# Kernel optimization log

Measured on AMD Instinct MI355X. Metric: run time of the kernel, lower is better.

## Reference

```python
import jax, jax.numpy as jnp
import numpy as np

B, S, D = 8, 4096, 1024
H, DH = 16, 64
DM = H * DH  # d_model = 1024


def setup_inputs() -> dict:
    key = jax.random.key(0)
    k0, k1, k2, k3 = jax.random.split(key, 4)
    x = jax.random.uniform(k0, (B, S, D), dtype=jnp.float32)
    # nn.Linear weights (stored here pre-transposed as [in, out]).
    Wq = jax.random.normal(k1, (D, DM), dtype=jnp.float32) * 0.02
    Wkv = jax.random.normal(k2, (D, 2 * DM), dtype=jnp.float32) * 0.02
    Wlin = jax.random.normal(k3, (DM, DM), dtype=jnp.float32) * 0.02
    blin = jnp.zeros((DM,), dtype=jnp.float32)
    return {"x": x, "Wq": Wq, "Wkv": Wkv, "Wlin": Wlin, "blin": blin}


def reference(x, Wq, Wkv, Wlin, blin):
    scale = DH ** (-0.5)
    # projections; cond_dim=None => cond = x (self attention), mask=None
    q = (x @ Wq).reshape(B, S, H, DH)          # [B,S,H,DH]
    kv = (x @ Wkv).reshape(B, S, H, 2 * DH)    # [B,S,H,2*DH]
    k, v = kv[..., :DH], kv[..., DH:]
    # dual softmax: q over feature dim (scaled), k over sequence dim
    q = jax.nn.softmax(q, axis=-1) * scale
    k = jax.nn.softmax(k, axis=1)              # seq axis in BSHD layout
    # context = k^T @ v per (batch, head): [B,H,DH,DH]
    context = jnp.einsum('bshd,bshe->bhde', k, v)
    # out = q @ context: [B,S,H,DH]
    out = jnp.einsum('bshd,bhde->bshe', q, context).reshape(B, S, DM)
    return out @ Wlin + blin
```

## Files before the change

### kernel.cpp

```cpp
#include <hip/hip_runtime.h>
#include <hip/hip_bf16.h>
#include <cstdint>

using bf16 = __hip_bfloat16;
typedef __attribute__((ext_vector_type(8))) short bf16x8;
typedef __attribute__((ext_vector_type(4))) float f32x4;

struct alignas(16) B8 { bf16 h[8]; };
struct alignas(8)  B4 { bf16 h[4]; };

__device__ __forceinline__ void gll16(const void* g, void* l) {
  __builtin_amdgcn_global_load_lds((__attribute__((address_space(1))) void*)g,
                                   (__attribute__((address_space(3))) void*)l,
                                   16, 0, 0);
}


__global__ __launch_bounds__(256) void cast_x_frag(const float* __restrict__ x,
                                                   bf16* __restrict__ xr) {
  __shared__ float tile[16][257];
  const int g = blockIdx.x;
  const int t = threadIdx.x;
  const float* src = x + (size_t)g * 16384;
  bf16* dst = xr + (size_t)g * 16384;
  const int r = t >> 4, cl = t & 15;
  for (int kp = 0; kp < 4; ++kp) {
    const int k0 = kp * 256;
    if (kp) __syncthreads();
    #pragma unroll
    for (int s = 0; s < 4; ++s) {
      const int c0 = cl * 4 + 64 * s;
      float4 v = *(const float4*)(src + (size_t)r * 1024 + k0 + c0);
      tile[r][c0 + 0] = v.x; tile[r][c0 + 1] = v.y;
      tile[r][c0 + 2] = v.z; tile[r][c0 + 3] = v.w;
    }
    __syncthreads();
    #pragma unroll
    for (int rd = 0; rd < 2; ++rd) {
      const int c = rd * 256 + t;
      const int ql = c >> 4, rr = c & 15;
      B8 o;
      #pragma unroll
      for (int jj = 0; jj < 8; ++jj) o.h[jj] = __float2bfloat16(tile[rr][ql * 8 + jj]);
      *(B8*)(dst + ((size_t)(kp * 32 + ql) * 16 + rr) * 8) = o;
    }
  }
}

__global__ __launch_bounds__(256) void wcast_frag(const float* __restrict__ W,
                                                  bf16* __restrict__ out,
                                                  int N, int n_glob0) {
  __shared__ float tw[256][17];
  const int k0 = blockIdx.x * 256;
  const int n0 = blockIdx.y * 16;
  const int t = threadIdx.x;
  {
    const int nn = t & 15, kk0 = t >> 4;
    #pragma unroll
    for (int s = 0; s < 16; ++s) {
      const int kk = kk0 + 16 * s;
      tw[kk][nn] = W[(size_t)(k0 + kk) * N + n0 + nn];
    }
  }
  __syncthreads();
  const int ng = (n_glob0 + n0) >> 4;
  #pragma unroll
  for (int rd = 0; rd < 2; ++rd) {
    const int c = rd * 256 + t;
    const int ql = c >> 4, r = c & 15;
    B8 o;
    #pragma unroll
    for (int jj = 0; jj < 8; ++jj) o.h[jj] = __float2bfloat16(tw[ql * 8 + jj][r]);
    *(B8*)(out + (((size_t)ng * 128 + (k0 >> 3) + ql) * 16 + r) * 8) = o;
  }
}

__global__ void tcast(const float* __restrict__ W, bf16* __restrict__ WT, int K, int N) {
  __shared__ float tile[32][33];
  int k0 = blockIdx.y * 32, n0 = blockIdx.x * 32;
  int tx = threadIdx.x, ty = threadIdx.y;
  for (int yy = ty; yy < 32; yy += 8)
    tile[yy][tx] = W[(size_t)(k0 + yy) * N + n0 + tx];
  __syncthreads();
  for (int yy = ty; yy < 32; yy += 8)
    WT[(size_t)(n0 + yy) * K + k0 + tx] = __float2bfloat16(tile[tx][yy]);
}

__device__ __forceinline__ void gemm_mainloop_256(
    const bf16* __restrict__ aop0, const bf16* __restrict__ aop1,
    const bf16* __restrict__ bop0, const bf16* __restrict__ bop1,
    bf16* ldsA, bf16* ldsB, int wd0, int wd1,
    int aoff, int boff, f32x4 (&acc)[8][4])
{
#define STAGE_A(slot, ko) do { gll16(aop0 + (ko) * 16, ldsA + (slot) * 8192 + wd0); \
                               gll16(aop1 + (ko) * 16, ldsA + (slot) * 8192 + wd1); } while (0)
#define STAGE_B(slot, ko) do { gll16(bop0 + (ko) * 16, ldsB + (slot) * 8192 + wd0); \
                               gll16(bop1 + (ko) * 16, ldsB + (slot) * 8192 + wd1); } while (0)
#define AFRAG(slot, i) (*(const bf16x8*)(ldsA + (slot) * 8192 + aoff + (i) * 512))
#define BFRAG(slot, j) (*(const bf16x8*)(ldsB + (slot) * 8192 + boff + (j) * 512))

  bf16x8 a1[4], a2[4], bb[2][4];

#define SECTION(S, CURB, NXTB, DO_PF, PFS, DO_ST, SLOT, KO)                         \
  do {                                                                              \
    asm volatile("s_waitcnt lgkmcnt(0)" ::: "memory");                              \
    __builtin_amdgcn_sched_barrier(0);                                              \
    __builtin_amdgcn_s_setprio(1);                                                  \
    _Pragma("unroll")                                                               \
    for (int i = 0; i < 4; i++) {                                                   \
      _Pragma("unroll")                                                             \
      for (int j = 0; j < 4; j++)                                                   \
        acc[i][j] = __builtin_amdgcn_mfma_f32_16x16x32_bf16(a1[i], bb[CURB][j],     \
                                                            acc[i][j], 0, 0, 0);    \
      a2[i] = AFRAG(S, i + 4);                                                      \
      if (DO_ST && i == 0) gll16(aop0 + (KO) * 16, ldsA + (SLOT) * 8192 + wd0);     \
      if (DO_ST && i == 1) gll16(aop1 + (KO) * 16, ldsA + (SLOT) * 8192 + wd1);     \
    }                                                                               \
    asm volatile("s_waitcnt lgkmcnt(0)" ::: "memory");                              \
    __builtin_amdgcn_sched_barrier(0);                                              \
    _Pragma("unroll")                                                               \
    for (int i = 0; i < 4; i++) {                                                   \
      _Pragma("unroll")                                                             \
      for (int j = 0; j < 4; j++)                                                   \
        acc[i + 4][j] = __builtin_amdgcn_mfma_f32_16x16x32_bf16(a2[i], bb[CURB][j], \
                                                                acc[i + 4][j], 0, 0, 0); \
      if (DO_PF) { bb[NXTB][i] = BFRAG(PFS, i); a1[i] = AFRAG(PFS, i); }            \
      if (DO_ST && i == 0) gll16(bop0 + (KO) * 16, ldsB + (SLOT) * 8192 + wd0);     \
      if (DO_ST && i == 1) gll16(bop1 + (KO) * 16, ldsB + (SLOT) * 8192 + wd1);     \
    }                                                                               \
    __builtin_amdgcn_s_setprio(0);                                                  \
  } while (0)

#define BOUNDARY(VMC)                                                               \
  do {                                                                              \
    asm volatile("s_waitcnt vmcnt(" #VMC ")" ::: "memory");                         \
    __builtin_amdgcn_s_barrier();                                                   \
    __builtin_amdgcn_sched_barrier(0);                                              \
  } while (0)

  STAGE_A(0, 0);  STAGE_B(0, 0);
  STAGE_A(1, 32); STAGE_B(1, 32);
  STAGE_A(2, 64); STAGE_B(2, 64);
  asm volatile("s_waitcnt vmcnt(4)" ::: "memory");
  __builtin_amdgcn_s_barrier();
  __builtin_amdgcn_sched_barrier(0);
  #pragma unroll
  for (int j = 0; j < 4; j++) bb[0][j] = BFRAG(0, j);
  #pragma unroll
  for (int i = 0; i < 4; i++) a1[i] = AFRAG(0, i);

  for (int q = 0; q < 7; ++q) {
    const int ko = q * 128;
    SECTION(0, 0, 1, true, 1, true, 3, ko + 96);
    BOUNDARY(4);
    SECTION(1, 1, 0, true, 2, true, 0, ko + 128);
    BOUNDARY(4);
    SECTION(2, 0, 1, true, 3, true, 1, ko + 160);
    BOUNDARY(4);
    SECTION(3, 1, 0, true, 0, true, 2, ko + 192);
    BOUNDARY(4);
  }
  SECTION(0, 0, 1, true, 1, true, 3, 992);
  BOUNDARY(4);
  SECTION(1, 1, 0, true, 2, false, 0, 0);
  BOUNDARY(0);
  SECTION(2, 0, 1, true, 3, false, 0, 0);
  BOUNDARY(0);
  SECTION(3, 1, 0, false, 0, false, 0, 0);

  __syncthreads();
#undef SECTION
#undef BOUNDARY
#undef STAGE_A
#undef STAGE_B
#undef AFRAG
#undef BFRAG
}

constexpr int QKV_NT = 12;

__global__ __launch_bounds__(512, 2)
void gemm_qkv(const bf16* __restrict__ A, const bf16* __restrict__ BT,
              bf16* __restrict__ Yq, float* __restrict__ ctxAcc)
{
  __shared__ __align__(16) union {
    struct { bf16 a[4 * 8192]; bf16 b[4 * 8192]; } g;
    struct { bf16 ekT[2][16384]; bf16 vT[2][16384]; } c;
  } sm;

  const int t = threadIdx.x;
  const int wave = t >> 6, lane = t & 63;
  const int lr = lane & 15, kq = lane >> 4;
  const int wm = wave >> 2, wn = wave & 3;
  const int bid = (int)blockIdx.x;
  const int swz = (bid & 7) * 192 + (bid >> 3);
  const int bm = swz / QKV_NT, bn = swz % QKV_NT;
  const int m0 = bm * 256, n0 = bn * 256;

  const bf16* aop0 = A + (size_t)((m0 >> 4) + wave) * 16384 + lane * 8;
  const bf16* aop1 = aop0 + 131072;
  const bf16* bop0 = BT + (size_t)((n0 >> 4) + wave) * 16384 + lane * 8;
  const bf16* bop1 = bop0 + 131072;
  const int wd0 = wave * 512;
  const int wd1 = 4096 + wave * 512;

  const int aoff = wm * 4096 + lane * 8;
  const int boff = wn * 2048 + lane * 8;

  const f32x4 zero = {0.f, 0.f, 0.f, 0.f};
  f32x4 acc[8][4];
  #pragma unroll
  for (int i = 0; i < 8; i++)
    #pragma unroll
    for (int j = 0; j < 4; j++) acc[i][j] = zero;

  gemm_mainloop_256(aop0, aop1, bop0, bop1, sm.g.a, sm.g.b, wd0, wd1,
                    aoff, boff, acc);

  if (bn < 4) {
    const int qb = (n0 + wn * 64) >> 3;
    const int jo = (lr >> 3) * 128;
    #pragma unroll
    for (int i = 0; i < 8; i++) {
      #pragma unroll
      for (int r = 0; r < 4; r++) {
        float m = fmaxf(fmaxf(acc[i][0][r], acc[i][1][r]),
                        fmaxf(acc[i][2][r], acc[i][3][r]));
        m = fmaxf(m, __shfl_xor(m, 1));
        m = fmaxf(m, __shfl_xor(m, 2));
        m = fmaxf(m, __shfl_xor(m, 4));
        m = fmaxf(m, __shfl_xor(m, 8));
        float ex[4]; float s = 0.f;
        #pragma unroll
        for (int j = 0; j < 4; j++) { ex[j] = __expf(acc[i][j][r] - m); s += ex[j]; }
        s += __shfl_xor(s, 1);
        s += __shfl_xor(s, 2);
        s += __shfl_xor(s, 4);
        s += __shfl_xor(s, 8);
        const float inv = 0.125f / s;
        const int row = m0 + wm * 128 + i * 16 + kq * 4 + r;
        bf16* yb = Yq + (((size_t)(row >> 4) * 128 + qb) * 16 + (row & 15)) * 8 + (lr & 7);
        #pragma unroll
        for (int j = 0; j < 4; j++)
          yb[j * 256 + jo] = __float2bfloat16(ex[j] * inv);
      }
    }
  } else {
    const int bb2 = m0 >> 12;
    const int h0 = (n0 - 1024) >> 7;
    const int hloc = wn >> 1, isV = wn & 1;
    bf16* const dstT = (isV ? sm.c.vT[hloc] : sm.c.ekT[hloc]);

    float zp[4] = {0.f, 0.f, 0.f, 0.f};
    #pragma unroll
    for (int i = 0; i < 8; i++) {
      const int sbase = wm * 128 + i * 16 + kq * 4;
      const int sxo = sbase >> 3;
      const int sby = (sbase & 7) * 2;
      #pragma unroll
      for (int j = 0; j < 4; j++) {
        const int d = j * 16 + lr;
        B4 pk;
        if (!isV) {
          #pragma unroll
          for (int r = 0; r < 4; r++) {
            float e = __expf(acc[i][j][r]);
            zp[j] += e;
            pk.h[r] = __float2bfloat16(e);
          }
        } else {
          #pragma unroll
          for (int r = 0; r < 4; r++) pk.h[r] = __float2bfloat16(acc[i][j][r]);
        }
        *(B4*)((char*)dstT + d * 512 + ((sxo ^ (d & 7)) << 4) + sby) = pk;
      }
    }

    if (!isV) {
      #pragma unroll
      for (int j = 0; j < 4; j++) {
        zp[j] += __shfl_xor(zp[j], 16);
        zp[j] += __shfl_xor(zp[j], 32);
      }
      if (kq == 0) {
        float* zb = ctxAcc + (size_t)(bb2 * 16 + h0 + hloc) * 4160 + 4096;
        #pragma unroll
        for (int j = 0; j < 4; j++) atomicAdd(zb + j * 16 + lr, zp[j]);
      }
    }
    __syncthreads();

    const int hh = wave >> 2, dq = wave & 3;
    const bf16* const ek = sm.c.ekT[hh];
    const bf16* const vv = sm.c.vT[hh];
    f32x4 racc[4] = {zero, zero, zero, zero};
    #pragma unroll
    for (int ks = 0; ks < 8; ks++) {
      const int ch = ks * 4 + kq;
      bf16x8 af = *(const bf16x8*)((const char*)ek + (dq * 16 + lr) * 512 + ((ch ^ (lr & 7)) << 4));
      #pragma unroll
      for (int j = 0; j < 4; j++) {
        bf16x8 bfr = *(const bf16x8*)((const char*)vv + (j * 16 + lr) * 512 + ((ch ^ (lr & 7)) << 4));
        racc[j] = __builtin_amdgcn_mfma_f32_16x16x32_bf16(af, bfr, racc[j], 0, 0, 0);
      }
    }
    float* cb = ctxAcc + (size_t)(bb2 * 16 + h0 + hh) * 4160;
    #pragma unroll
    for (int j = 0; j < 4; j++) {
      #pragma unroll
      for (int r = 0; r < 4; r++)
        atomicAdd(cb + (dq * 16 + kq * 4 + r) * 64 + j * 16 + lr, racc[j][r]);
    }
  }
}

__global__ __launch_bounds__(256) void make_w2t(const float* __restrict__ ctxAcc,
                                                const bf16* __restrict__ WlinT,
                                                bf16* __restrict__ W2T) {
  const int nc = blockIdx.x;
  const int bh = blockIdx.y;
  const int b = bh >> 4, h = bh & 15;
  const int t = threadIdx.x, lane = t & 63, w = t >> 6;
  const float* src = ctxAcc + (size_t)bh * 4160;
  const float invz = 1.0f / src[4096 + lane];
  float creg[64];
  const float* crow = src + lane * 64;
  #pragma unroll
  for (int e4 = 0; e4 < 16; e4++) {
    float4 v = *(const float4*)(crow + e4 * 4);
    creg[e4 * 4 + 0] = v.x * invz; creg[e4 * 4 + 1] = v.y * invz;
    creg[e4 * 4 + 2] = v.z * invz; creg[e4 * 4 + 3] = v.w * invz;
  }
  for (int i = 0; i < 16; i++) {
    const int n = nc * 64 + w * 16 + i;
    const bf16* wrow = WlinT + (size_t)n * 1024 + h * 64;
    float acc = 0.f;
    #pragma unroll
    for (int e8 = 0; e8 < 8; e8++) {
      B8 v = *(const B8*)(wrow + e8 * 8);
      #pragma unroll
      for (int j = 0; j < 8; j++) acc += creg[e8 * 8 + j] * __bfloat162float(v.h[j]);
    }
    W2T[(size_t)b * 1048576 +
        (((size_t)(n >> 4) * 128 + h * 8 + (lane >> 3)) * 16 + (n & 15)) * 8 + (lane & 7)]
        = __float2bfloat16(acc);
  }
}

__global__ __launch_bounds__(512, 2)
void gemm_out(const bf16* __restrict__ Aall, const bf16* __restrict__ BTall,
              float* __restrict__ Call, const float* __restrict__ bias)
{
  __shared__ __align__(16) struct { bf16 a[4 * 8192]; bf16 b[4 * 8192]; } sm;
  const int t = threadIdx.x;
  const int wave = t >> 6, lane = t & 63;
  const int lr = lane & 15, kq = lane >> 4;
  const int wm = wave >> 2, wn = wave & 3;
  const int bid = (int)blockIdx.x;
  const int swz = (bid & 7) * 64 + (bid >> 3);
  const int bz = swz >> 6;
  const int r  = swz & 63;
  const int bm = r >> 2, bn = r & 3;
  const int m0 = bm * 256, n0 = bn * 256;
  const bf16* A  = Aall  + (size_t)bz * 4194304;
  const bf16* BT = BTall + (size_t)bz * 1048576;
  float* C       = Call  + (size_t)bz * 4194304;

  const bf16* aop0 = A + (size_t)((m0 >> 4) + wave) * 16384 + lane * 8;
  const bf16* aop1 = aop0 + 131072;
  const bf16* bop0 = BT + (size_t)((n0 >> 4) + wave) * 16384 + lane * 8;
  const bf16* bop1 = bop0 + 131072;
  const int wd0 = wave * 512;
  const int wd1 = 4096 + wave * 512;

  const int aoff = wm * 4096 + lane * 8;
  const int boff = wn * 2048 + lane * 8;

  const f32x4 zero = {0.f, 0.f, 0.f, 0.f};
  f32x4 acc[8][4];
  #pragma unroll
  for (int i = 0; i < 8; i++)
    #pragma unroll
    for (int j = 0; j < 4; j++) acc[i][j] = zero;

  gemm_mainloop_256(aop0, aop1, bop0, bop1, sm.a, sm.b, wd0, wd1,
                    aoff, boff, acc);

  float bv[4];
  #pragma unroll
  for (int j = 0; j < 4; j++) bv[j] = bias[n0 + wn * 64 + j * 16 + lr];
  #pragma unroll
  for (int i = 0; i < 8; i++) {
    const int row0 = m0 + wm * 128 + i * 16 + kq * 4;
    #pragma unroll
    for (int j = 0; j < 4; j++) {
      const int col = n0 + wn * 64 + j * 16 + lr;
      const float bvj = bv[j];
      #pragma unroll
      for (int r2 = 0; r2 < 4; r2++)
        C[(size_t)(row0 + r2) * 1024 + col] = acc[i][j][r2] + bvj;
    }
  }
}

extern "C" void kernel_launch(void* const* d_in, const int* in_sizes, int n_in,
                              void* d_out, int out_size, void* d_ws, size_t ws_size,
                              hipStream_t stream) {
  (void)in_sizes; (void)n_in; (void)out_size; (void)ws_size;
  const float* x    = (const float*)d_in[0];
  const float* Wq   = (const float*)d_in[1];
  const float* Wkv  = (const float*)d_in[2];
  const float* Wlin = (const float*)d_in[3];
  const float* blin = (const float*)d_in[4];
  float* out = (float*)d_out;

  bf16* x_bf  = (bf16*)d_ws;
  bf16* WTc   = x_bf + 33554432;
  bf16* WlinT = WTc + 3145728;
  bf16* Yq    = WlinT + 1048576;
  bf16* W2T   = Yq + 33554432;
  float* ctxAcc = (float*)(W2T + 8388608);

  cast_x_frag<<<2048, 256, 0, stream>>>(x, x_bf);
  wcast_frag<<<dim3(4, 64), 256, 0, stream>>>(Wq, WTc, 1024, 0);
  wcast_frag<<<dim3(4, 128), 256, 0, stream>>>(Wkv, WTc, 2048, 1024);
  tcast<<<dim3(32, 32), dim3(32, 8), 0, stream>>>(Wlin, WlinT, 1024, 1024);

  hipMemsetAsync(ctxAcc, 0, (size_t)128 * 4160 * sizeof(float), stream);

  gemm_qkv<<<dim3(128 * QKV_NT), 512, 0, stream>>>(x_bf, WTc, Yq, ctxAcc);
  make_w2t<<<dim3(16, 128), 256, 0, stream>>>(ctxAcc, WlinT, W2T);
  gemm_out<<<dim3(512), 512, 0, stream>>>(Yq, W2T, out, blin);
}
```

Baseline: 370.2 us.

## Load GEMM B fragments directly from global into registers, bypassing LDS

The shared GEMM mainloop no longer stages the B operand through LDS. Each wave now reads its B fragments straight from global memory into registers, one K-step ahead, and the vmcnt waits are adjusted to cover these loads. This halves LDS use and removes B's LDS traffic, which could allow more occupancy. In exchange, the four waves sharing each N-column re-read B from global/L2, and B-load latency now sits in the MFMA pipeline with only one step of lookahead.

New measurement: 368.2 us. About the same (-0.5%).

```diff
diff --git a/kernel.cpp b/kernel.cpp
--- a/kernel.cpp
+++ b/kernel.cpp
@@ -88,20 +88,17 @@
 
 __device__ __forceinline__ void gemm_mainloop_256(
     const bf16* __restrict__ aop0, const bf16* __restrict__ aop1,
-    const bf16* __restrict__ bop0, const bf16* __restrict__ bop1,
-    bf16* ldsA, bf16* ldsB, int wd0, int wd1,
-    int aoff, int boff, f32x4 (&acc)[8][4])
+    const bf16* __restrict__ bfp,
+    bf16* ldsA, int wd0, int wd1, int aoff, f32x4 (&acc)[8][4])
 {
 #define STAGE_A(slot, ko) do { gll16(aop0 + (ko) * 16, ldsA + (slot) * 8192 + wd0); \
                                gll16(aop1 + (ko) * 16, ldsA + (slot) * 8192 + wd1); } while (0)
-#define STAGE_B(slot, ko) do { gll16(bop0 + (ko) * 16, ldsB + (slot) * 8192 + wd0); \
-                               gll16(bop1 + (ko) * 16, ldsB + (slot) * 8192 + wd1); } while (0)
 #define AFRAG(slot, i) (*(const bf16x8*)(ldsA + (slot) * 8192 + aoff + (i) * 512))
-#define BFRAG(slot, j) (*(const bf16x8*)(ldsB + (slot) * 8192 + boff + (j) * 512))
+#define BGLOB(j, ko) (*(const bf16x8*)(bfp + (size_t)(j) * 16384 + (ko) * 16))
 
   bf16x8 a1[4], a2[4], bb[2][4];
 
-#define SECTION(S, CURB, NXTB, DO_PF, PFS, DO_ST, SLOT, KO)                         \
+#define SECTION(S, CURB, NXTB, DO_PFB, BKO, DO_PF, PFS, DO_ST, SLOT, KO)            \
   do {                                                                              \
     asm volatile("s_waitcnt lgkmcnt(0)" ::: "memory");                              \
     __builtin_amdgcn_sched_barrier(0);                                              \
@@ -115,6 +112,7 @@
       a2[i] = AFRAG(S, i + 4);                                                      \
       if (DO_ST && i == 0) gll16(aop0 + (KO) * 16, ldsA + (SLOT) * 8192 + wd0);     \
       if (DO_ST && i == 1) gll16(aop1 + (KO) * 16, ldsA + (SLOT) * 8192 + wd1);     \
+      if (DO_PFB) bb[NXTB][i] = BGLOB(i, BKO);                                      \
     }                                                                               \
     asm volatile("s_waitcnt lgkmcnt(0)" ::: "memory");                              \
     __builtin_amdgcn_sched_barrier(0);                                              \
@@ -124,9 +122,7 @@
       for (int j = 0; j < 4; j++)                                                   \
         acc[i + 4][j] = __builtin_amdgcn_mfma_f32_16x16x32_bf16(a2[i], bb[CURB][j], \
                                                                 acc[i + 4][j], 0, 0, 0); \
-      if (DO_PF) { bb[NXTB][i] = BFRAG(PFS, i); a1[i] = AFRAG(PFS, i); }            \
-      if (DO_ST && i == 0) gll16(bop0 + (KO) * 16, ldsB + (SLOT) * 8192 + wd0);     \
-      if (DO_ST && i == 1) gll16(bop1 + (KO) * 16, ldsB + (SLOT) * 8192 + wd1);     \
+      if (DO_PF) { a1[i] = AFRAG(PFS, i); }                                         \
     }                                                                               \
     __builtin_amdgcn_s_setprio(0);                                                  \
   } while (0)
@@ -138,43 +134,41 @@
     __builtin_amdgcn_sched_barrier(0);                                              \
   } while (0)
 
-  STAGE_A(0, 0);  STAGE_B(0, 0);
-  STAGE_A(1, 32); STAGE_B(1, 32);
-  STAGE_A(2, 64); STAGE_B(2, 64);
+  STAGE_A(0, 0); STAGE_A(1, 32); STAGE_A(2, 64);
+  #pragma unroll
+  for (int j = 0; j < 4; j++) bb[0][j] = BGLOB(j, 0);
   asm volatile("s_waitcnt vmcnt(4)" ::: "memory");
   __builtin_amdgcn_s_barrier();
   __builtin_amdgcn_sched_barrier(0);
   #pragma unroll
-  for (int j = 0; j < 4; j++) bb[0][j] = BFRAG(0, j);
-  #pragma unroll
   for (int i = 0; i < 4; i++) a1[i] = AFRAG(0, i);
 
   for (int q = 0; q < 7; ++q) {
     const int ko = q * 128;
-    SECTION(0, 0, 1, true, 1, true, 3, ko + 96);
-    BOUNDARY(4);
-    SECTION(1, 1, 0, true, 2, true, 0, ko + 128);
-    BOUNDARY(4);
-    SECTION(2, 0, 1, true, 3, true, 1, ko + 160);
-    BOUNDARY(4);
-    SECTION(3, 1, 0, true, 0, true, 2, ko + 192);
-    BOUNDARY(4);
-  }
-  SECTION(0, 0, 1, true, 1, true, 3, 992);
-  BOUNDARY(4);
-  SECTION(1, 1, 0, true, 2, false, 0, 0);
-  BOUNDARY(0);
-  SECTION(2, 0, 1, true, 3, false, 0, 0);
-  BOUNDARY(0);
-  SECTION(3, 1, 0, false, 0, false, 0, 0);
-
+    SECTION(0, 0, 1, true, ko + 32,  true, 1, true, 3, ko + 96);
+    BOUNDARY(6);
+    SECTION(1, 1, 0, true, ko + 64,  true, 2, true, 0, ko + 128);
+    BOUNDARY(6);
+    SECTION(2, 0, 1, true, ko + 96,  true, 3, true, 1, ko + 160);
+    BOUNDARY(6);
+    SECTION(3, 1, 0, true, ko + 128, true, 0, true, 2, ko + 192);
+    BOUNDARY(6);
+  }
+  SECTION(0, 0, 1, true, 928, true, 1, true, 3, 992);
+  BOUNDARY(6);
+  SECTION(1, 1, 0, true, 960, true, 2, false, 0, 0);
+  BOUNDARY(6);
+  SECTION(2, 0, 1, true, 992, true, 3, false, 0, 0);
+  BOUNDARY(6);
+  SECTION(3, 1, 0, false, 0, false, 0, false, 0, 0);
+
+  asm volatile("s_waitcnt vmcnt(0)" ::: "memory");
   __syncthreads();
 #undef SECTION
 #undef BOUNDARY
 #undef STAGE_A
-#undef STAGE_B
 #undef AFRAG
-#undef BFRAG
+#undef BGLOB
 }
 
 constexpr int QKV_NT = 12;
@@ -184,7 +178,7 @@
               bf16* __restrict__ Yq, float* __restrict__ ctxAcc)
 {
   __shared__ __align__(16) union {
-    struct { bf16 a[4 * 8192]; bf16 b[4 * 8192]; } g;
+    struct { bf16 a[4 * 8192]; } g;
     struct { bf16 ekT[2][16384]; bf16 vT[2][16384]; } c;
   } sm;
 
@@ -199,13 +193,10 @@
 
   const bf16* aop0 = A + (size_t)((m0 >> 4) + wave) * 16384 + lane * 8;
   const bf16* aop1 = aop0 + 131072;
-  const bf16* bop0 = BT + (size_t)((n0 >> 4) + wave) * 16384 + lane * 8;
-  const bf16* bop1 = bop0 + 131072;
+  const bf16* bfp = BT + (size_t)((n0 >> 4) + wn * 4) * 16384 + lane * 8;
   const int wd0 = wave * 512;
   const int wd1 = 4096 + wave * 512;
-
   const int aoff = wm * 4096 + lane * 8;
-  const int boff = wn * 2048 + lane * 8;
 
   const f32x4 zero = {0.f, 0.f, 0.f, 0.f};
   f32x4 acc[8][4];
@@ -214,8 +205,7 @@
     #pragma unroll
     for (int j = 0; j < 4; j++) acc[i][j] = zero;
 
-  gemm_mainloop_256(aop0, aop1, bop0, bop1, sm.g.a, sm.g.b, wd0, wd1,
-                    aoff, boff, acc);
+  gemm_mainloop_256(aop0, aop1, bfp, sm.g.a, wd0, wd1, aoff, acc);
 
   if (bn < 4) {
     const int qb = (n0 + wn * 64) >> 3;
@@ -351,7 +341,7 @@
 void gemm_out(const bf16* __restrict__ Aall, const bf16* __restrict__ BTall,
               float* __restrict__ Call, const float* __restrict__ bias)
 {
-  __shared__ __align__(16) struct { bf16 a[4 * 8192]; bf16 b[4 * 8192]; } sm;
+  __shared__ __align__(16) struct { bf16 a[4 * 8192]; } sm;
   const int t = threadIdx.x;
   const int wave = t >> 6, lane = t & 63;
   const int lr = lane & 15, kq = lane >> 4;
@@ -368,13 +358,10 @@
 
   const bf16* aop0 = A + (size_t)((m0 >> 4) + wave) * 16384 + lane * 8;
   const bf16* aop1 = aop0 + 131072;
-  const bf16* bop0 = BT + (size_t)((n0 >> 4) + wave) * 16384 + lane * 8;
-  const bf16* bop1 = bop0 + 131072;
+  const bf16* bfp = BT + (size_t)((n0 >> 4) + wn * 4) * 16384 + lane * 8;
   const int wd0 = wave * 512;
   const int wd1 = 4096 + wave * 512;
-
   const int aoff = wm * 4096 + lane * 8;
-  const int boff = wn * 2048 + lane * 8;
 
   const f32x4 zero = {0.f, 0.f, 0.f, 0.f};
   f32x4 acc[8][4];
@@ -383,8 +370,7 @@
     #pragma unroll
     for (int j = 0; j < 4; j++) acc[i][j] = zero;
 
-  gemm_mainloop_256(aop0, aop1, bop0, bop1, sm.a, sm.b, wd0, wd1,
-                    aoff, boff, acc);
+  gemm_mainloop_256(aop0, aop1, bfp, sm.a, wd0, wd1, aoff, acc);
 
   float bv[4];
   #pragma unroll
```
